# Optimization experiments

Hardware: AMD Instinct MI355X
Metric: run time of the kernel (lower is better)

The kernel has to match this reference:

```python
import jax, jax.numpy as jnp
import numpy as np

B, L, CIN, COUT, TEMB, N_MODES = 32, 8192, 64, 64, 256, 64
M = N_MODES // 2 + 1  # retained rfft modes = 33
EPS = 1e-5


def setup_inputs() -> dict:
    key = jax.random.key(0)
    ks = jax.random.split(key, 12)
    std_w = float(np.sqrt(1.0 / (2.0 * CIN)))
    # flax Dense default kernel init = lecun_normal ~ normal(std=1/sqrt(fan_in)); plain normal is fine for a reference
    return {
        "x": jax.random.normal(ks[0], (B, L, CIN), jnp.float32),
        "t_emb": jax.random.normal(ks[1], (B, TEMB), jnp.float32),
        # SpectralFreqTimeConv1D params
        "spec_w_real": jax.random.normal(ks[2], (M, CIN, COUT), jnp.float32) * std_w,
        "spec_w_imag": jax.random.normal(ks[3], (M, CIN, COUT), jnp.float32) * std_w,
        "dense_re": jax.random.normal(ks[4], (TEMB, M), jnp.float32) / np.sqrt(TEMB),
        "dense_im": jax.random.normal(ks[5], (TEMB, M), jnp.float32) / np.sqrt(TEMB),
        # TimeConv1D params
        "conv_kernel": jax.random.normal(ks[6], (CIN, COUT), jnp.float32) / np.sqrt(CIN),
        "conv_bias": jnp.zeros((COUT,), jnp.float32),
        "tc_weights": jax.random.normal(ks[7], (COUT, COUT), jnp.float32) * 0.01,  # nn.initializers.normal() stddev=0.01
        "psi_kernel": jax.random.normal(ks[8], (TEMB, 2 * COUT), jnp.float32) / np.sqrt(TEMB),
        # BatchNorm params
        "bn_scale": jnp.ones((COUT,), jnp.float32),
        "bn_bias": jnp.zeros((COUT,), jnp.float32),
    }


def reference(x, t_emb, spec_w_real, spec_w_imag, dense_re, dense_im,
              conv_kernel, conv_bias, tc_weights, psi_kernel, bn_scale, bn_bias):
    b, L_in, _ = x.shape
    n_freq = L_in // 2 + 1

    # ---- SpectralFreqTimeConv1D ----
    x_ft = jnp.fft.rfft(x, axis=-2, norm="forward")            # (b, n_freq, CIN) complex
    t_c = (t_emb @ dense_re) + 1j * (t_emb @ dense_im)         # (b, M) complex
    W = spec_w_real + 1j * spec_w_imag                          # (M, CIN, COUT) complex
    # diagonal-in-mode modulation: equivalent to the eye-based einsum chain
    out_m = t_c[:, :, None] * jnp.einsum("bmi,mio->bmo", x_ft[:, :M, :], W)  # (b, M, COUT)
    out_ft = jnp.zeros((b, n_freq, COUT), jnp.complex64).at[:, :M, :].set(out_m)
    x_spec = jnp.fft.irfft(out_ft, axis=-2, n=L_in, norm="forward")  # (b, L, COUT)

    # ---- TimeConv1D (residual branch) ----
    h = x @ conv_kernel + conv_bias                             # 1x1 conv: (b, L, COUT)
    psi = t_emb @ psi_kernel                                    # (b, 2*COUT)
    w_t, b_t = jnp.split(psi, 2, axis=-1)
    # einsum('ij,bjk,blk->bli', W, diag(w_t), h) == (h * w_t) @ W^T
    x_res = jnp.einsum("blj,ij->bli", h * w_t[:, None, :], tc_weights) + b_t[:, None, :]

    # ---- combine, batchnorm (training: batch stats), activation ----
    out = x_spec + x_res
    mean = out.mean(axis=(0, 1))
    var = out.var(axis=(0, 1))
    out = (out - mean) * jax.lax.rsqrt(var + EPS) * bn_scale + bn_bias
    return jax.nn.relu(out)
```

## Files before the change

### kernel.cpp

```cpp
#include <hip/hip_runtime.h>
#include <hip/hip_fp16.h>

typedef short short8 __attribute__((ext_vector_type(8)));
typedef float f32x4 __attribute__((ext_vector_type(4)));
typedef unsigned int u32;
typedef u32 u32x4 __attribute__((ext_vector_type(4)));
typedef unsigned short u16;

#define BB 32
#define LL 8192
#define TE 256
#define MM 33
#define INVL (1.0f/8192.0f)

#define VTB_OFF  589824
#define DD_OFF   720896
#define DD2_OFF  722944
#define BNP_OFF  731200

#define SRED2_OFF 4227072
#define VF_OFF    4491264

static __device__ __forceinline__ u16 f2b(float f) {
  u32 u = __float_as_uint(f);
  return (u16)((u + 0x7FFFu + ((u >> 16) & 1u)) >> 16);
}
static __device__ __forceinline__ u32 pk2(float lo, float hi) {
  return __builtin_amdgcn_perm(__float_as_uint(hi) + 0x8000u,
                               __float_as_uint(lo) + 0x8000u,
                               0x07060302u);
}
static __device__ __forceinline__ float fsin(float rev) {
  float r; asm("v_sin_f32 %0, %1" : "=v"(r) : "v"(rev)); return r;
}
static __device__ __forceinline__ float fcos(float rev) {
  float r; asm("v_cos_f32 %0, %1" : "=v"(r) : "v"(rev)); return r;
}
static __device__ __forceinline__ u16 tval(int m, bool is_sin, int l) {
  float rev = (float)((m * l) & (LL - 1)) * INVL;
  return f2b(is_sin ? fsin(rev) : fcos(rev));
}
static __device__ __forceinline__ u16 tslotj(int j, int l) {
  int m = (j == 0) ? 32 : (j <= 32 ? j : j - 32);
  bool is_sin = (j == 0) || (j >= 33);
  return tval(m, is_sin, l);
}

__global__ __launch_bounds__(512) void k_dft(const float* __restrict__ x,
                                             float* __restrict__ scr) {
  __shared__ __align__(16) u16 sX[2][64 * 136];
  __shared__ float sOnes[8 * 64];
  int tid = threadIdx.x;
  int b = blockIdx.x >> 5, chunk = blockIdx.x & 31;
  int l0 = chunk * 256;
  int w = tid >> 6, lane = tid & 63;

  f32x4 acc[4];
#pragma unroll
  for (int ct = 0; ct < 4; ++ct) acc[ct] = (f32x4){0.f, 0.f, 0.f, 0.f};

  int arow = lane & 15;
  int kb = (lane >> 4) * 8;
  bool isg = (w >= 4);
  int gi = w - 4;
  int sc = tid & 63, lg = tid >> 6;

  int jrow = w * 16 + arow;
  int m_slot = (jrow == 0) ? 32 : (jrow <= 32 ? jrow : jrow - 32);
  bool is_sin = (jrow == 0) || (jrow >= 33);

  float vx[16];
  float psum = 0.f;
#pragma unroll
  for (int i = 0; i < 16; ++i)
    vx[i] = x[(b * LL + l0 + lg * 16 + i) * 64 + sc];
  {
    u32 wv[8];
#pragma unroll
    for (int j = 0; j < 8; ++j) {
      wv[j] = pk2(vx[2 * j], vx[2 * j + 1]);
      psum += vx[2 * j] + vx[2 * j + 1];
    }
    u32x4* dst = (u32x4*)&sX[0][sc * 136 + lg * 16];
    dst[0] = (u32x4){wv[0], wv[1], wv[2], wv[3]};
    dst[1] = (u32x4){wv[4], wv[5], wv[6], wv[7]};
  }
  __syncthreads();

#pragma unroll
  for (int i = 0; i < 16; ++i)
    vx[i] = x[(b * LL + l0 + 128 + lg * 16 + i) * 64 + sc];

#pragma unroll
  for (int kk = 0; kk < 4; ++kk) {
    short8 a;
    if (isg) {
      a = *reinterpret_cast<const short8*>(&sX[0][(gi * 16 + arow) * 136 + kk * 32 + kb]);
    } else {
      union { short8 s; u32 wv[4]; } A;
      int lb = l0 + kk * 32 + kb;
#pragma unroll
      for (int p2 = 0; p2 < 4; ++p2)
        A.wv[p2] = (u32)tval(m_slot, is_sin, lb + 2 * p2) |
                   ((u32)tval(m_slot, is_sin, lb + 2 * p2 + 1) << 16);
      a = A.s;
    }
#pragma unroll
    for (int ct = 0; ct < 4; ++ct) {
      short8 bf = *reinterpret_cast<const short8*>(&sX[0][(ct * 16 + arow) * 136 + kk * 32 + kb]);
      acc[ct] = __builtin_amdgcn_mfma_f32_16x16x32_bf16(a, bf, acc[ct], 0, 0, 0);
    }
  }

  {
    u32 wv[8];
#pragma unroll
    for (int j = 0; j < 8; ++j) {
      wv[j] = pk2(vx[2 * j], vx[2 * j + 1]);
      psum += vx[2 * j] + vx[2 * j + 1];
    }
    u32x4* dst = (u32x4*)&sX[1][sc * 136 + lg * 16];
    dst[0] = (u32x4){wv[0], wv[1], wv[2], wv[3]};
    dst[1] = (u32x4){wv[4], wv[5], wv[6], wv[7]};
  }
  sOnes[tid] = psum;
  __syncthreads();

#pragma unroll
  for (int kk = 0; kk < 4; ++kk) {
    short8 a;
    if (isg) {
      a = *reinterpret_cast<const short8*>(&sX[1][(gi * 16 + arow) * 136 + kk * 32 + kb]);
    } else {
      union { short8 s; u32 wv[4]; } A;
      int lb = l0 + 128 + kk * 32 + kb;
#pragma unroll
      for (int p2 = 0; p2 < 4; ++p2)
        A.wv[p2] = (u32)tval(m_slot, is_sin, lb + 2 * p2) |
                   ((u32)tval(m_slot, is_sin, lb + 2 * p2 + 1) << 16);
      a = A.s;
    }
#pragma unroll
    for (int ct = 0; ct < 4; ++ct) {
      short8 bf = *reinterpret_cast<const short8*>(&sX[1][(ct * 16 + arow) * 136 + kk * 32 + kb]);
      acc[ct] = __builtin_amdgcn_mfma_f32_16x16x32_bf16(a, bf, acc[ct], 0, 0, 0);
    }
  }

  int rowbase = isg ? (65 + gi * 16) : (w * 16);
  int rowb = (lane >> 4) * 4;
  u16* pp = (u16*)scr + (size_t)(b * 32 + chunk) * 129 * 64;
#pragma unroll
  for (int ct = 0; ct < 4; ++ct) {
    int col = ct * 16 + (lane & 15);
#pragma unroll
    for (int r = 0; r < 4; ++r)
      pp[(rowbase + rowb + r) * 64 + col] = __half_as_ushort(__float2half(acc[ct][r]));
  }
  if (tid < 64) {
    float s = 0.f;
#pragma unroll
    for (int g = 0; g < 8; ++g) s += sOnes[g * 64 + tid];
    pp[64 * 64 + tid] = __half_as_ushort(__float2half(s));
  }
}

__global__ __launch_bounds__(256) void k_red1(float* __restrict__ scr) {
  int bid = blockIdx.x, tid = threadIdx.x;
  int b = bid / 17, rx = bid % 17;
  int p = rx * 256 + tid;
  if (p >= 4128) return;
  const u32* pb = (const u32*)scr + (size_t)b * 32 * 4128;
  float a0 = 0.f, a1 = 0.f;
#pragma unroll 8
  for (int ch = 0; ch < 32; ++ch) {
    u32 u = pb[ch * 4128 + p];
    __half2 h2 = *reinterpret_cast<const __half2*>(&u);
    float2 f = __half22float2(h2);
    a0 += f.x; a1 += f.y;
  }
  *reinterpret_cast<float2*>(scr + SRED2_OFF + b * 8256 + 2 * p) =
      make_float2(a0, a1);
}

__global__ __launch_bounds__(256) void k_vb(
    const float* __restrict__ t_emb, const float* __restrict__ dre,
    const float* __restrict__ dim_, const float* __restrict__ pk,
    const float* __restrict__ swr, const float* __restrict__ swi,
    const float* __restrict__ ck, const float* __restrict__ cbias,
    const float* __restrict__ tw, float* __restrict__ scr,
    float* __restrict__ ws) {
  __shared__ float smem[12352];
  int tid = threadIdx.x;

  if (blockIdx.x < 33) {
    int m = blockIdx.x;
    float2* sW = (float2*)smem;
    float2* sX = (float2*)(smem + 8192);
    float* sTcb = smem + 8192 + 4096;

    for (int idx = tid; idx < 8192; idx += 256) smem[idx] = t_emb[idx];
    __syncthreads();
    if (tid < 64) {
      int b = tid & 31;
      const float* dd = (tid < 32) ? dre : dim_;
      float a = 0.f;
#pragma unroll 8
      for (int j = 0; j < TE; ++j) a = fmaf(smem[b * 256 + j], dd[j * MM + m], a);
      sTcb[tid] = a;
    }
    __syncthreads();

    for (int idx = tid; idx < 4096; idx += 256)
      sW[idx] = make_float2(swr[m * 4096 + idx], swi[m * 4096 + idx]);
    for (int idx = tid; idx < 2048; idx += 256) {
      int b = idx >> 6, i = idx & 63;
      const float* sr = scr + SRED2_OFF + b * 8256;
      float xr, xi;
      if (m == 0)      { xr = sr[64 * 64 + i] * INVL;  xi = 0.f; }
      else if (m < 32) { xr = sr[m * 64 + i] * INVL;   xi = -sr[(32 + m) * 64 + i] * INVL; }
      else             { xr = sr[32 * 64 + i] * INVL;  xi = -sr[0 * 64 + i] * INVL; }
      sX[idx] = make_float2(xr, xi);
    }
    __syncthreads();

    int w = tid >> 6, lane = tid & 63;
    for (int p = 0; p < 8; ++p) {
      int b = p * 4 + w;
      float a0 = 0.f, a1 = 0.f, a2 = 0.f, a3 = 0.f;
#pragma unroll 16
      for (int i = 0; i < 64; ++i) {
        float2 wv = sW[i * 64 + lane];
        float2 xv = sX[b * 64 + i];
        a0 = fmaf(xv.x, wv.x, a0);
        a1 = fmaf(xv.y, wv.y, a1);
        a2 = fmaf(xv.x, wv.y, a2);
        a3 = fmaf(xv.y, wv.x, a3);
      }
      float ar = a0 - a1, ai = a2 + a3;
      float tcr = sTcb[b], tci = sTcb[32 + b];
      float cr = tcr * ar - tci * ai;
      float ci = tcr * ai + tci * ar;
      if (m == 0) {
        ws[DD2_OFF + b * 64 + lane] = cr;
      } else {
        float crr = 2.f * cr, cii = -2.f * ci;
        int js = (m == 32) ? 0 : 32 + m;
        u16* vtb = (u16*)ws + VTB_OFF * 2 + (b * 64 + lane) * 128;
        vtb[64 + m] = f2b(crr);
        vtb[64 + js] = f2b(cii);
        float* vf = scr + VF_OFF + b * 8192;
        vf[(64 + m) * 64 + lane] = crr;
        vf[(64 + js) * 64 + lane] = cii;
      }
    }
  } else {
    int b = blockIdx.x - 33;
    float* sCkT = smem;
    float* sPtw = smem + 4096;
    float* sTe  = smem + 8192;
    float* sPsi = smem + 8448;

    sTe[tid] = t_emb[b * 256 + tid];
    __syncthreads();
    if (tid < 128) {
      float a = 0.f;
#pragma unroll 8
      for (int j = 0; j < TE; ++j) a = fmaf(sTe[j], pk[j * 128 + tid], a);
      sPsi[tid] = a;
    }
    __syncthreads();
    for (int idx = tid; idx < 4096; idx += 256) {
      int c = idx >> 6, j = idx & 63;
      sCkT[j * 64 + c] = ck[idx];
      sPtw[idx] = sPsi[j] * tw[idx];
    }
    __syncthreads();

    u16* vtb = (u16*)ws + VTB_OFF * 2 + b * 64 * 128;
    float* vf = scr + VF_OFF + b * 8192;
    int lane = tid & 63, w = tid >> 6;
#pragma unroll 4
    for (int it = 0; it < 16; ++it) {
      int o = it * 4 + w;
      float a = 0.f;
#pragma unroll 16
      for (int j = 0; j < 64; ++j)
        a = fmaf(sCkT[j * 64 + lane], sPtw[o * 64 + j], a);
      vtb[o * 128 + lane] = f2b(a);
      vf[lane * 64 + o] = a;
    }
    if (tid < 64) {
      float a = 0.f;
      for (int j = 0; j < 64; ++j) a = fmaf(cbias[j], sPtw[tid * 64 + j], a);
      ws[DD_OFF + b * 64 + tid] = a + sPsi[64 + tid];
    }
  }
}

__global__ __launch_bounds__(256) void k_bn(const float* __restrict__ scr,
                                            float* __restrict__ ws) {
  __shared__ float sVx[64 * 64];
  __shared__ float sGx[64 * 64];
  __shared__ float sS[64 * 64];
  __shared__ float sSum[64];
  __shared__ float sP[4][2][64];
  int tid = threadIdx.x, b = blockIdx.x;
  const float* sr = scr + SRED2_OFF + b * 8256;
  const float* vf = scr + VF_OFF + b * 8192;

  for (int p = tid; p < 4096; p += 256) {
    sVx[p] = vf[p];
    sGx[p] = sr[65 * 64 + p];
    sS[p]  = sr[p];
  }
  if (tid < 64) sSum[tid] = sr[64 * 64 + tid];
  __syncthreads();

  int o = tid & 63, part = tid >> 6;
  float m1 = 0.f, q1 = 0.f, cross = 0.f, vt2 = 0.f;
  for (int ii = 0; ii < 16; ++ii) {
    int i = part * 16 + ii;
    float vx = sVx[i * 64 + o];
    m1 = fmaf(sSum[i], vx, m1);
    float w0 = 0.f, w1 = 0.f, c0 = 0.f, c1 = 0.f;
#pragma unroll
    for (int j = 0; j < 64; j += 2) {
      float va = sVx[j * 64 + o], vb = sVx[(j + 1) * 64 + o];
      w0 = fmaf(sGx[i * 64 + j], va, w0);
      w1 = fmaf(sGx[i * 64 + j + 1], vb, w1);
      c0 = fmaf(sS[i * 64 + j], va, c0);
      c1 = fmaf(sS[i * 64 + j + 1], vb, c1);
    }
    q1 = fmaf(vx, w0 + w1, q1);
    float vt = vf[(64 + i) * 64 + o];
    vt2 = fmaf(vt, vt, vt2);
    cross = fmaf(vt, c0 + c1, cross);
  }
  sP[part][0][o] = m1;
  sP[part][1][o] = q1 + 2.f * cross + 4096.f * vt2;
  __syncthreads();
  if (tid < 64) {
    float m = sP[0][0][tid] + sP[1][0][tid] + sP[2][0][tid] + sP[3][0][tid];
    float q = sP[0][1][tid] + sP[1][1][tid] + sP[2][1][tid] + sP[3][1][tid];
    float D = ws[DD_OFF + b * 64 + tid] + ws[DD2_OFF + b * 64 + tid];
    ws[BNP_OFF + b * 128 + tid]      = m + 8192.f * D;
    ws[BNP_OFF + b * 128 + 64 + tid] = q + 2.f * D * m + 8192.f * D * D;
  }
}

__global__ __launch_bounds__(256) void k_main(const float* __restrict__ x,
                                              const float* __restrict__ ws,
                                              const float* __restrict__ bns,
                                              const float* __restrict__ bnb,
                                              float* __restrict__ out) {
  __shared__ float sD[64];
  __shared__ float sA[64];
  __shared__ float sB[64];
  __shared__ float sPp[4][64];
  __shared__ float sPq[4][64];
  int tid = threadIdx.x, w = tid >> 6, lane = tid & 63;
  int b = blockIdx.x >> 6, rg = blockIdx.x & 63;
  const u16* wsu = (const u16*)ws;

  int kb = (lane >> 4) * 8;
  const u16* vtb = wsu + VTB_OFF * 2 + b * 64 * 128;
  short8 bf[4][4];
#pragma unroll
  for (int kk = 0; kk < 4; ++kk)
#pragma unroll
    for (int ct = 0; ct < 4; ++ct)
      bf[kk][ct] = *reinterpret_cast<const short8*>(
          vtb + (ct * 16 + (lane & 15)) * 128 + kk * 32 + kb);

  {
    int o = tid & 63, g = tid >> 6;
    float pm = 0.f, pq = 0.f;
#pragma unroll
    for (int r = 0; r < 8; ++r) {
      int bb = g * 8 + r;
      pm += ws[BNP_OFF + bb * 128 + o];
      pq += ws[BNP_OFF + bb * 128 + 64 + o];
    }
    sPp[g][o] = pm;
    sPq[g][o] = pq;
  }
  if (tid < 64) sD[tid] = ws[DD_OFF + b * 64 + tid] + ws[DD2_OFF + b * 64 + tid];
  __syncthreads();
  if (tid < 64) {
    const float inv_n = 1.f / (32.f * 8192.f);
    float mean = (sPp[0][tid] + sPp[1][tid] + sPp[2][tid] + sPp[3][tid]) * inv_n;
    float ex2  = (sPq[0][tid] + sPq[1][tid] + sPq[2][tid] + sPq[3][tid]) * inv_n;
    float var = ex2 - mean * mean;
    float istd = rsqrtf(var + 1e-5f);
    float al = istd * bns[tid];
    sA[tid] = al;
    sB[tid] = bnb[tid] - mean * al;
  }
  __syncthreads();

  int rowb = (lane >> 4) * 4;
  int lbase = rg * 128 + w * 32;

#pragma unroll
  for (int rt = 0; rt < 2; ++rt) {
    int l = lbase + rt * 16 + (lane & 15);
    const float* xq = x + (b * LL + l) * 64;
    float4 u0 = *reinterpret_cast<const float4*>(xq + kb);
    float4 u1 = *reinterpret_cast<const float4*>(xq + kb + 4);
    float4 u2 = *reinterpret_cast<const float4*>(xq + 32 + kb);
    float4 u3 = *reinterpret_cast<const float4*>(xq + 32 + kb + 4);
    union { short8 s; u32 wv[4]; } A0, A1, A2, A3;
    A0.wv[0] = pk2(u0.x, u0.y); A0.wv[1] = pk2(u0.z, u0.w);
    A0.wv[2] = pk2(u1.x, u1.y); A0.wv[3] = pk2(u1.z, u1.w);
    A1.wv[0] = pk2(u2.x, u2.y); A1.wv[1] = pk2(u2.z, u2.w);
    A1.wv[2] = pk2(u3.x, u3.y); A1.wv[3] = pk2(u3.z, u3.w);
#pragma unroll
    for (int p2 = 0; p2 < 4; ++p2) {
      A2.wv[p2] = (u32)tslotj(kb + 2 * p2, l) |
                  ((u32)tslotj(kb + 2 * p2 + 1, l) << 16);
      A3.wv[p2] = (u32)tslotj(32 + kb + 2 * p2, l) |
                  ((u32)tslotj(32 + kb + 2 * p2 + 1, l) << 16);
    }

    f32x4 acc[4];
#pragma unroll
    for (int ct = 0; ct < 4; ++ct) acc[ct] = (f32x4){0.f, 0.f, 0.f, 0.f};
#pragma unroll
    for (int ct = 0; ct < 4; ++ct) {
      acc[ct] = __builtin_amdgcn_mfma_f32_16x16x32_bf16(A0.s, bf[0][ct], acc[ct], 0, 0, 0);
      acc[ct] = __builtin_amdgcn_mfma_f32_16x16x32_bf16(A1.s, bf[1][ct], acc[ct], 0, 0, 0);
      acc[ct] = __builtin_amdgcn_mfma_f32_16x16x32_bf16(A2.s, bf[2][ct], acc[ct], 0, 0, 0);
      acc[ct] = __builtin_amdgcn_mfma_f32_16x16x32_bf16(A3.s, bf[3][ct], acc[ct], 0, 0, 0);
    }
#pragma unroll
    for (int ct = 0; ct < 4; ++ct) {
      int o = ct * 16 + (lane & 15);
      float dd = sD[o], al = sA[o], be = sB[o];
#pragma unroll
      for (int r = 0; r < 4; ++r) {
        float v = acc[ct][r] + dd;
        out[(b * LL + lbase + rt * 16 + rowb + r) * 64 + o] =
            fmaxf(fmaf(v, al, be), 0.f);
      }
    }
  }
}

extern "C" void kernel_launch(void* const* d_in, const int* in_sizes, int n_in,
                              void* d_out, int out_size, void* d_ws, size_t ws_size,
                              hipStream_t stream) {
  const float* x     = (const float*)d_in[0];
  const float* t_emb = (const float*)d_in[1];
  const float* swr   = (const float*)d_in[2];
  const float* swi   = (const float*)d_in[3];
  const float* dre   = (const float*)d_in[4];
  const float* dim_  = (const float*)d_in[5];
  const float* ck    = (const float*)d_in[6];
  const float* cbias = (const float*)d_in[7];
  const float* tw    = (const float*)d_in[8];
  const float* pk    = (const float*)d_in[9];
  const float* bns   = (const float*)d_in[10];
  const float* bnb   = (const float*)d_in[11];
  float* ws  = (float*)d_ws;
  float* out = (float*)d_out;

  k_dft<<<1024, 512, 0, stream>>>(x, out);
  k_red1<<<544, 256, 0, stream>>>(out);
  k_vb<<<65, 256, 0, stream>>>(t_emb, dre, dim_, pk, swr, swi,
                               ck, cbias, tw, out, ws);
  k_bn<<<32, 256, 0, stream>>>(out, ws);
  k_main<<<2048, 256, 0, stream>>>(x, ws, bns, bnb, out);
}
```

Before: 90.66 us.

## Split DFT chunks into 128-sample blocks of 256 threads with two tiles per wave

The DFT kernel now runs 2048 blocks of 256 threads. Each block covers 128 positions instead of 256, and each wave computes two 16-row output tiles. The in-kernel two-stage double-buffered load/compute overlap is dropped. Partial sums per batch double to 64 chunks, so the reduction kernel reads twice as many fp16 partials and the scratch offsets move. This aims to raise occupancy and block-level parallelism, at the cost of more partial-sum traffic in k_red1 and lost intra-block overlap.

```diff
diff --git a/kernel.cpp b/kernel.cpp
--- a/kernel.cpp
+++ b/kernel.cpp
@@ -18,8 +18,8 @@
 #define DD2_OFF  722944
 #define BNP_OFF  731200
 
-#define SRED2_OFF 4227072
-#define VF_OFF    4491264
+#define SRED2_OFF 8454144
+#define VF_OFF    8718336
 
 static __device__ __forceinline__ u16 f2b(float f) {
   u32 u = __float_as_uint(f);
@@ -46,121 +46,85 @@
   return tval(m, is_sin, l);
 }
 
-__global__ __launch_bounds__(512) void k_dft(const float* __restrict__ x,
+__global__ __launch_bounds__(256) void k_dft(const float* __restrict__ x,
                                              float* __restrict__ scr) {
-  __shared__ __align__(16) u16 sX[2][64 * 136];
-  __shared__ float sOnes[8 * 64];
+  __shared__ __align__(16) u16 sX[64 * 136];
+  __shared__ float sOnes[4 * 64];
   int tid = threadIdx.x;
-  int b = blockIdx.x >> 5, chunk = blockIdx.x & 31;
-  int l0 = chunk * 256;
+  int b = blockIdx.x >> 6, chunk = blockIdx.x & 63;
+  int l0 = chunk * 128;
   int w = tid >> 6, lane = tid & 63;
-
-  f32x4 acc[4];
-#pragma unroll
-  for (int ct = 0; ct < 4; ++ct) acc[ct] = (f32x4){0.f, 0.f, 0.f, 0.f};
-
   int arow = lane & 15;
   int kb = (lane >> 4) * 8;
-  bool isg = (w >= 4);
-  int gi = w - 4;
   int sc = tid & 63, lg = tid >> 6;
 
-  int jrow = w * 16 + arow;
-  int m_slot = (jrow == 0) ? 32 : (jrow <= 32 ? jrow : jrow - 32);
-  bool is_sin = (jrow == 0) || (jrow >= 33);
-
-  float vx[16];
   float psum = 0.f;
 #pragma unroll
-  for (int i = 0; i < 16; ++i)
-    vx[i] = x[(b * LL + l0 + lg * 16 + i) * 64 + sc];
-  {
-    u32 wv[8];
-#pragma unroll
-    for (int j = 0; j < 8; ++j) {
+  for (int half = 0; half < 4; ++half) {
+    int lp0 = lg * 32 + half * 8;
+    float vx[8];
+#pragma unroll
+    for (int i = 0; i < 8; ++i)
+      vx[i] = x[(b * LL + l0 + lp0 + i) * 64 + sc];
+    u32 wv[4];
+#pragma unroll
+    for (int j = 0; j < 4; ++j) {
       wv[j] = pk2(vx[2 * j], vx[2 * j + 1]);
       psum += vx[2 * j] + vx[2 * j + 1];
     }
-    u32x4* dst = (u32x4*)&sX[0][sc * 136 + lg * 16];
-    dst[0] = (u32x4){wv[0], wv[1], wv[2], wv[3]};
-    dst[1] = (u32x4){wv[4], wv[5], wv[6], wv[7]};
-  }
-  __syncthreads();
-
-#pragma unroll
-  for (int i = 0; i < 16; ++i)
-    vx[i] = x[(b * LL + l0 + 128 + lg * 16 + i) * 64 + sc];
-
-#pragma unroll
-  for (int kk = 0; kk < 4; ++kk) {
-    short8 a;
-    if (isg) {
-      a = *reinterpret_cast<const short8*>(&sX[0][(gi * 16 + arow) * 136 + kk * 32 + kb]);
-    } else {
-      union { short8 s; u32 wv[4]; } A;
-      int lb = l0 + kk * 32 + kb;
-#pragma unroll
-      for (int p2 = 0; p2 < 4; ++p2)
-        A.wv[p2] = (u32)tval(m_slot, is_sin, lb + 2 * p2) |
-                   ((u32)tval(m_slot, is_sin, lb + 2 * p2 + 1) << 16);
-      a = A.s;
-    }
-#pragma unroll
-    for (int ct = 0; ct < 4; ++ct) {
-      short8 bf = *reinterpret_cast<const short8*>(&sX[0][(ct * 16 + arow) * 136 + kk * 32 + kb]);
-      acc[ct] = __builtin_amdgcn_mfma_f32_16x16x32_bf16(a, bf, acc[ct], 0, 0, 0);
-    }
-  }
-
-  {
-    u32 wv[8];
-#pragma unroll
-    for (int j = 0; j < 8; ++j) {
-      wv[j] = pk2(vx[2 * j], vx[2 * j + 1]);
-      psum += vx[2 * j] + vx[2 * j + 1];
-    }
-    u32x4* dst = (u32x4*)&sX[1][sc * 136 + lg * 16];
-    dst[0] = (u32x4){wv[0], wv[1], wv[2], wv[3]};
-    dst[1] = (u32x4){wv[4], wv[5], wv[6], wv[7]};
+    *(u32x4*)&sX[sc * 136 + lp0] = (u32x4){wv[0], wv[1], wv[2], wv[3]};
   }
   sOnes[tid] = psum;
   __syncthreads();
 
-#pragma unroll
-  for (int kk = 0; kk < 4; ++kk) {
-    short8 a;
-    if (isg) {
-      a = *reinterpret_cast<const short8*>(&sX[1][(gi * 16 + arow) * 136 + kk * 32 + kb]);
-    } else {
-      union { short8 s; u32 wv[4]; } A;
-      int lb = l0 + 128 + kk * 32 + kb;
-#pragma unroll
-      for (int p2 = 0; p2 < 4; ++p2)
-        A.wv[p2] = (u32)tval(m_slot, is_sin, lb + 2 * p2) |
-                   ((u32)tval(m_slot, is_sin, lb + 2 * p2 + 1) << 16);
-      a = A.s;
-    }
+  bool isg = (w >= 2);
+  u16* pp = (u16*)scr + (size_t)(b * 64 + chunk) * 129 * 64;
+  int rowb = (lane >> 4) * 4;
+
+#pragma unroll
+  for (int tt = 0; tt < 2; ++tt) {
+    int tile = (isg ? (w - 2) : w) * 2 + tt;
+    int jrow = tile * 16 + arow;
+    int m_slot = (jrow == 0) ? 32 : (jrow <= 32 ? jrow : jrow - 32);
+    bool is_sin = (jrow == 0) || (jrow >= 33);
+
+    f32x4 acc[4];
+#pragma unroll
+    for (int ct = 0; ct < 4; ++ct) acc[ct] = (f32x4){0.f, 0.f, 0.f, 0.f};
+
+#pragma unroll
+    for (int kk = 0; kk < 4; ++kk) {
+      short8 a;
+      if (isg) {
+        a = *reinterpret_cast<const short8*>(&sX[jrow * 136 + kk * 32 + kb]);
+      } else {
+        union { short8 s; u32 wv[4]; } A;
+        int lb = l0 + kk * 32 + kb;
+#pragma unroll
+        for (int p2 = 0; p2 < 4; ++p2)
+          A.wv[p2] = (u32)tval(m_slot, is_sin, lb + 2 * p2) |
+                     ((u32)tval(m_slot, is_sin, lb + 2 * p2 + 1) << 16);
+        a = A.s;
+      }
+#pragma unroll
+      for (int ct = 0; ct < 4; ++ct) {
+        short8 bf = *reinterpret_cast<const short8*>(&sX[(ct * 16 + arow) * 136 + kk * 32 + kb]);
+        acc[ct] = __builtin_amdgcn_mfma_f32_16x16x32_bf16(a, bf, acc[ct], 0, 0, 0);
+      }
+    }
+
+    int rowbase = (isg ? 65 : 0) + tile * 16;
 #pragma unroll
     for (int ct = 0; ct < 4; ++ct) {
-      short8 bf = *reinterpret_cast<const short8*>(&sX[1][(ct * 16 + arow) * 136 + kk * 32 + kb]);
-      acc[ct] = __builtin_amdgcn_mfma_f32_16x16x32_bf16(a, bf, acc[ct], 0, 0, 0);
-    }
-  }
-
-  int rowbase = isg ? (65 + gi * 16) : (w * 16);
-  int rowb = (lane >> 4) * 4;
-  u16* pp = (u16*)scr + (size_t)(b * 32 + chunk) * 129 * 64;
-#pragma unroll
-  for (int ct = 0; ct < 4; ++ct) {
-    int col = ct * 16 + (lane & 15);
-#pragma unroll
-    for (int r = 0; r < 4; ++r)
-      pp[(rowbase + rowb + r) * 64 + col] = __half_as_ushort(__float2half(acc[ct][r]));
-  }
+      int col = ct * 16 + (lane & 15);
+#pragma unroll
+      for (int r = 0; r < 4; ++r)
+        pp[(rowbase + rowb + r) * 64 + col] = __half_as_ushort(__float2half(acc[ct][r]));
+    }
+  }
+
   if (tid < 64) {
-    float s = 0.f;
-#pragma unroll
-    for (int g = 0; g < 8; ++g) s += sOnes[g * 64 + tid];
+    float s = sOnes[tid] + sOnes[64 + tid] + sOnes[128 + tid] + sOnes[192 + tid];
     pp[64 * 64 + tid] = __half_as_ushort(__float2half(s));
   }
 }
@@ -170,10 +134,10 @@
   int b = bid / 17, rx = bid % 17;
   int p = rx * 256 + tid;
   if (p >= 4128) return;
-  const u32* pb = (const u32*)scr + (size_t)b * 32 * 4128;
+  const u32* pb = (const u32*)scr + (size_t)b * 64 * 4128;
   float a0 = 0.f, a1 = 0.f;
 #pragma unroll 8
-  for (int ch = 0; ch < 32; ++ch) {
+  for (int ch = 0; ch < 64; ++ch) {
     u32 u = pb[ch * 4128 + p];
     __half2 h2 = *reinterpret_cast<const __half2*>(&u);
     float2 f = __half22float2(h2);
@@ -465,7 +429,7 @@
   float* ws  = (float*)d_ws;
   float* out = (float*)d_out;
 
-  k_dft<<<1024, 512, 0, stream>>>(x, out);
+  k_dft<<<2048, 256, 0, stream>>>(x, out);
   k_red1<<<544, 256, 0, stream>>>(out);
   k_vb<<<65, 256, 0, stream>>>(t_emb, dre, dim_, pk, swr, swi,
                                ck, cbias, tw, out, ws);
```

Measured after the change: 95.48 us. 5.3% more time.
